# Optimization experiments

Measured on AMD Instinct MI355X. Metric: run time of the kernel, lower is better.

Reference implementation:

```python
import jax, jax.numpy as jnp
import numpy as np

SLOPE = 25.0   # fast_sigmoid surrogate slope (affects backward only)
THRESH = 1.0   # snntorch Leaky default threshold

@jax.custom_vjp
def spike(x):
    # Heaviside forward, fast-sigmoid surrogate backward
    return (x > 0).astype(x.dtype)

def _spike_fwd(x):
    return spike(x), x

def _spike_bwd(x, g):
    return (g / (SLOPE * jnp.abs(x) + 1.0) ** 2,)

spike.defvjp(_spike_fwd, _spike_bwd)


def setup_inputs() -> dict:
    key = jax.random.key(0)
    ks = jax.random.split(key, 16)
    B, T, F = 512, 1024, 64
    SNN, H, HOR = 128, 128, 24
    s = 0.05
    inp = {
        "x": jax.random.normal(ks[0], (B, T, F), jnp.float32),
        "proj_w": jax.random.normal(ks[1], (SNN, F), jnp.float32) * s,
        "proj_b": jnp.zeros((SNN,), jnp.float32),
        "beta1": jnp.full((SNN,), 0.9, jnp.float32),
        "beta2": jnp.full((SNN,), 0.9, jnp.float32),
        "gru_w_ih": jax.random.normal(ks[2], (3 * H, F + SNN), jnp.float32) * s,
        "gru_w_hh": jax.random.normal(ks[3], (3 * H, H), jnp.float32) * s,
        "gru_b_ih": jnp.zeros((3 * H,), jnp.float32),
        "gru_b_hh": jnp.zeros((3 * H,), jnp.float32),
        "attn_w1": jax.random.normal(ks[4], (H // 2, H), jnp.float32) * s,
        "attn_b1": jnp.zeros((H // 2,), jnp.float32),
        "attn_w2": jax.random.normal(ks[5], (1, H // 2), jnp.float32) * s,
        "attn_b2": jnp.zeros((1,), jnp.float32),
        "head_w": jax.random.normal(ks[6], (HOR, H), jnp.float32) * s,
        "head_b": jnp.zeros((HOR,), jnp.float32),
    }
    return inp


def reference(x, proj_w, proj_b, beta1, beta2,
              gru_w_ih, gru_w_hh, gru_b_ih, gru_b_hh,
              attn_w1, attn_b1, attn_w2, attn_b2, head_w, head_b):
    b1 = jnp.clip(beta1, 0.0, 0.99)
    b2 = jnp.clip(beta2, 0.0, 0.99)

    delta = x[:, 1:, :] - x[:, :-1, :]   # (B, T-1, F)
    raw = x[:, 1:, :]
    h_s = delta @ proj_w.T + proj_b      # (B, T-1, SNN)

    B = x.shape[0]
    SNN = proj_w.shape[0]

    # snntorch Leaky (subtract reset, reset from previous step's spike):
    # mem_t = beta*mem_{t-1} + in_t - spk_{t-1}*thr ; spk_t = H(mem_t - thr)
    def snn_step(carry, inp_t):
        m1, s1, m2, s2 = carry
        m1 = b1 * m1 + inp_t - s1 * THRESH
        s1n = spike(m1 - THRESH)
        m2 = b2 * m2 + s1n - s2 * THRESH
        s2n = spike(m2 - THRESH)
        return (m1, s1n, m2, s2n), m2

    z = jnp.zeros((B, SNN), x.dtype)
    _, mem_rec = jax.lax.scan(snn_step, (z, z, z, z), jnp.swapaxes(h_s, 0, 1))
    h_snn = jnp.swapaxes(mem_rec, 0, 1)             # (B, T-1, SNN)

    h_comb = jnp.concatenate([raw, h_snn], axis=-1)  # (B, T-1, F+SNN)

    # GRU (PyTorch gate layout: r, z, n)
    H = gru_w_hh.shape[1]
    x_proj = h_comb @ gru_w_ih.T + gru_b_ih          # (B, T-1, 3H)

    def gru_step(h, xp):
        gh = h @ gru_w_hh.T + gru_b_hh
        xr, xz, xn = jnp.split(xp, 3, axis=-1)
        hr, hz, hn = jnp.split(gh, 3, axis=-1)
        r = jax.nn.sigmoid(xr + hr)
        zg = jax.nn.sigmoid(xz + hz)
        n = jnp.tanh(xn + r * hn)
        h_new = (1.0 - zg) * n + zg * h
        return h_new, h_new

    h0 = jnp.zeros((B, H), x.dtype)
    _, gru_seq = jax.lax.scan(gru_step, h0, jnp.swapaxes(x_proj, 0, 1))
    gru_out = jnp.swapaxes(gru_seq, 0, 1)            # (B, T-1, H)

    # Temporal attention over time (dim=1)
    scores = jax.nn.relu(gru_out @ attn_w1.T + attn_b1) @ attn_w2.T + attn_b2  # (B, T-1, 1)
    w = jax.nn.softmax(scores, axis=1)
    h_ann = (w * gru_out).sum(axis=1)                # (B, H)

    return h_ann @ head_w.T + head_b                 # (B, horizon)
```

## Files before the change

### kernel.cpp

```cpp
#include <hip/hip_runtime.h>

typedef unsigned short u16;
typedef __attribute__((ext_vector_type(8))) short short8;
typedef __attribute__((ext_vector_type(4))) float f32x4;

__device__ __forceinline__ u16 f2bf(float f) {
  union { float f; unsigned u; } v; v.f = f;
  unsigned r = v.u + 0x7fffu + ((v.u >> 16) & 1u);
  return (u16)(r >> 16);
}
__device__ __forceinline__ u16 truncbf(float f) {
  union { float f; unsigned u; } v; v.f = f;
  return (u16)(v.u >> 16);
}
__device__ __forceinline__ float bf2f(u16 h) {
  union { unsigned u; float f; } v; v.u = ((unsigned)h) << 16;
  return v.f;
}
__device__ __forceinline__ void gll16(const void* g, void* l) {
  __builtin_amdgcn_global_load_lds((const __attribute__((address_space(1))) unsigned*)g,
                                   (__attribute__((address_space(3))) unsigned*)l, 16, 0, 0);
}
__device__ __forceinline__ void bar_lds() {
  asm volatile("s_waitcnt lgkmcnt(0)" ::: "memory");
  __builtin_amdgcn_s_barrier();
  asm volatile("" ::: "memory");
}

#define BATCH 512
#define TS 1023
#define NF 64
#define NS 128
#define NH 128
#define NG 384
#define NC 192
#define CH 128

__global__ void k_prep(const float* __restrict__ wih, const float* __restrict__ w1,
                       u16* __restrict__ wihb, u16* __restrict__ w1b) {
  int i = blockIdx.x * 256 + threadIdx.x;
  if (i < NG * NC) wihb[i] = f2bf(wih[i]);
  if (i < 64 * NH) w1b[i] = f2bf(w1[i]);
}

__global__ __launch_bounds__(256, 2) void k_front(const float* __restrict__ x,
                                                  const float* __restrict__ pw,
                                                  const float* __restrict__ pb,
                                                  const float* __restrict__ beta1,
                                                  const float* __restrict__ beta2,
                                                  u16* __restrict__ hcomb) {
  __shared__ float hst[64 * 138];
  const int tid = threadIdx.x, lane = tid & 63, w = tid >> 6;
  const int m16 = lane & 15, quad = lane >> 4;
  const int b = blockIdx.x;
  const float* xb = x + (long)b * 65536;

  const int tm = (w >> 1) * 32, nn = (w & 1) * 64;

  short8 bh[2][4], bl[2][4];
  #pragma unroll
  for (int kc = 0; kc < 2; ++kc)
    #pragma unroll
    for (int ni = 0; ni < 4; ++ni) {
      const float* src = pw + (nn + ni * 16 + m16) * 64 + kc * 32 + quad * 8;
      f32x4 v0 = *(const f32x4*)src;
      f32x4 v1 = *(const f32x4*)(src + 4);
      #pragma unroll
      for (int jj = 0; jj < 8; ++jj) {
        float v = (jj < 4) ? v0[jj & 3] : v1[jj & 3];
        u16 hh = truncbf(v);
        bh[kc][ni][jj] = (short)hh;
        bl[kc][ni][jj] = (short)f2bf(v - bf2f(hh));
      }
    }

  float b1v = 0.f, b2v = 0.f, m1 = 0.f, s1 = 0.f, m2 = 0.f, s2 = 0.f;
  if (tid < 128) {
    b1v = fminf(fmaxf(beta1[tid], 0.f), 0.99f);
    b2v = fminf(fmaxf(beta2[tid], 0.f), 0.99f);
  }
  float pbv[4];
  #pragma unroll
  for (int ni = 0; ni < 4; ++ni) pbv[ni] = pb[nn + ni * 16 + m16];

  for (int tile = 0; tile < 16; ++tile) {
    const int t0 = tile * 64;
    const int tl = (TS - t0 < 64) ? (TS - t0) : 64;

    f32x4 acc[2][4] = {};
    #pragma unroll
    for (int kc = 0; kc < 2; ++kc) {
      short8 ah[2], al[2];
      #pragma unroll
      for (int mi = 0; mi < 2; ++mi) {
        int row = tm + mi * 16 + m16;
        int tA = t0 + row; if (tA > 1022) tA = 1022;
        const float* p0 = xb + (long)tA * 64 + kc * 32 + quad * 8;
        f32x4 lo0 = *(const f32x4*)p0;
        f32x4 lo1 = *(const f32x4*)(p0 + 4);
        f32x4 hi0 = *(const f32x4*)(p0 + 64);
        f32x4 hi1 = *(const f32x4*)(p0 + 68);
        float d[8];
        #pragma unroll
        for (int jj = 0; jj < 4; ++jj) { d[jj] = hi0[jj] - lo0[jj]; d[4 + jj] = hi1[jj] - lo1[jj]; }
        #pragma unroll
        for (int jj = 0; jj < 8; ++jj) {
          u16 hh = truncbf(d[jj]);
          ah[mi][jj] = (short)hh;
          al[mi][jj] = (short)f2bf(d[jj] - bf2f(hh));
        }
      }
      #pragma unroll
      for (int mi = 0; mi < 2; ++mi)
        #pragma unroll
        for (int ni = 0; ni < 4; ++ni) {
          acc[mi][ni] = __builtin_amdgcn_mfma_f32_16x16x32_bf16(ah[mi], bh[kc][ni], acc[mi][ni], 0, 0, 0);
          acc[mi][ni] = __builtin_amdgcn_mfma_f32_16x16x32_bf16(ah[mi], bl[kc][ni], acc[mi][ni], 0, 0, 0);
          acc[mi][ni] = __builtin_amdgcn_mfma_f32_16x16x32_bf16(al[mi], bh[kc][ni], acc[mi][ni], 0, 0, 0);
        }
    }
    #pragma unroll
    for (int mi = 0; mi < 2; ++mi)
      #pragma unroll
      for (int ni = 0; ni < 4; ++ni)
        #pragma unroll
        for (int rr = 0; rr < 4; ++rr)
          hst[(tm + mi * 16 + quad * 4 + rr) * 138 + nn + ni * 16 + m16] = acc[mi][ni][rr] + pbv[ni];
    bar_lds();
    if (tid < 128) {
      const int n = tid;
      u16* dst = hcomb + ((long)t0 * 512 + b) * NC + 64 + n;
      for (int tt = 0; tt < tl; tt += 8) {
        float v[8];
        #pragma unroll
        for (int jj = 0; jj < 8; ++jj) {
          int t = tt + jj; if (t > 63) t = 63;
          v[jj] = hst[t * 138 + n];
        }
        #pragma unroll
        for (int jj = 0; jj < 8; ++jj) {
          int t = tt + jj;
          if (t < tl) {
            m1 = b1v * m1 + v[jj] - s1;
            s1 = (m1 > 1.0f) ? 1.0f : 0.0f;
            m2 = b2v * m2 + s1 - s2;
            s2 = (m2 > 1.0f) ? 1.0f : 0.0f;
            dst[(long)t * (512 * NC)] = f2bf(m2);
          }
        }
      }
    } else {
      const int f = tid & 63, half = (tid >> 6) & 1;
      for (int r = half; r < tl; r += 2)
        hcomb[((long)(t0 + r) * 512 + b) * NC + f] = f2bf(xb[(long)(t0 + r + 1) * 64 + f]);
    }
    bar_lds();
  }
}

__device__ __forceinline__ void xproj_body(long row0, int n0, const u16* __restrict__ hc,
                                           const u16* __restrict__ wih, const float* __restrict__ bih,
                                           u16* __restrict__ xp, u16* As, u16* Bs) {
  const int tid = threadIdx.x, lane = tid & 63, w = tid >> 6;
  const int m16 = lane & 15, quad = lane >> 4;
  const int wm = (w >> 1) * 64, wn = (w & 1) * 64;
  f32x4 acc[4][4] = {};
  const char* gA = (const char*)hc + (row0 + (lane >> 2)) * (NC * 2) + (lane & 3) * 16;
  const char* gB = (const char*)wih + (long)(n0 + (lane >> 2)) * (NC * 2) + (lane & 3) * 16;
  for (int kc = 0; kc < 6; ++kc) {
    #pragma unroll
    for (int i = 0; i < 2; ++i) {
      int q = i * 4 + w;
      gll16(gA + (long)q * 16 * (NC * 2) + kc * 64, (char*)As + q * 1024);
      gll16(gB + (long)q * 16 * (NC * 2) + kc * 64, (char*)Bs + q * 1024);
    }
    __syncthreads();
    short8 af[4], bfr[4];
    #pragma unroll
    for (int mi = 0; mi < 4; ++mi) af[mi] = *(const short8*)((const char*)As + (wm + mi * 16 + m16) * 64 + quad * 16);
    #pragma unroll
    for (int ni = 0; ni < 4; ++ni) bfr[ni] = *(const short8*)((const char*)Bs + (wn + ni * 16 + m16) * 64 + quad * 16);
    #pragma unroll
    for (int mi = 0; mi < 4; ++mi)
      #pragma unroll
      for (int ni = 0; ni < 4; ++ni)
        acc[mi][ni] = __builtin_amdgcn_mfma_f32_16x16x32_bf16(af[mi], bfr[ni], acc[mi][ni], 0, 0, 0);
    __syncthreads();
  }
  #pragma unroll
  for (int ni = 0; ni < 4; ++ni) {
    int n = n0 + wn + ni * 16 + m16;
    float bias = bih[n];
    #pragma unroll
    for (int mi = 0; mi < 4; ++mi) {
      long r = row0 + wm + mi * 16 + quad * 4;
      #pragma unroll
      for (int rr = 0; rr < 4; ++rr)
        xp[(r + rr) * NG + n] = f2bf(acc[mi][ni][rr] + bias);
    }
  }
}

__global__ __launch_bounds__(256) void k_xproj(const u16* __restrict__ hc, const u16* __restrict__ wih,
                                               const float* __restrict__ bih, u16* __restrict__ xp) {
  __shared__ alignas(16) u16 As[4096], Bs[4096];
  xproj_body((long)blockIdx.x * 128, blockIdx.y * 128, hc, wih, bih, xp, As, Bs);
}

__device__ __forceinline__ void score_body(long row0, const u16* __restrict__ gbf, const u16* __restrict__ w1,
                                           const float* __restrict__ b1, const float* __restrict__ w2,
                                           const float* __restrict__ b2, float* __restrict__ scores,
                                           u16* Gs, u16* Ws) {
  const int tid = threadIdx.x, lane = tid & 63, w = tid >> 6;
  const int m16 = lane & 15, quad = lane >> 4;
  f32x4 acc[2][4] = {};
  const char* gG = (const char*)gbf + (row0 + (lane >> 2)) * (NH * 2) + (lane & 3) * 16;
  const char* gW = (const char*)w1 + (long)(w * 16 + (lane >> 2)) * (NH * 2) + (lane & 3) * 16;
  for (int kc = 0; kc < 4; ++kc) {
    #pragma unroll
    for (int i = 0; i < 2; ++i) {
      int q = i * 4 + w;
      gll16(gG + (long)q * 16 * (NH * 2) + kc * 64, (char*)Gs + q * 1024);
    }
    gll16(gW + kc * 64, (char*)Ws + w * 1024);
    __syncthreads();
    short8 af[2], bfr[4];
    #pragma unroll
    for (int mi = 0; mi < 2; ++mi) af[mi] = *(const short8*)((const char*)Gs + (w * 32 + mi * 16 + m16) * 64 + quad * 16);
    #pragma unroll
    for (int ni = 0; ni < 4; ++ni) bfr[ni] = *(const short8*)((const char*)Ws + (ni * 16 + m16) * 64 + quad * 16);
    #pragma unroll
    for (int mi = 0; mi < 2; ++mi)
      #pragma unroll
      for (int ni = 0; ni < 4; ++ni)
        acc[mi][ni] = __builtin_amdgcn_mfma_f32_16x16x32_bf16(af[mi], bfr[ni], acc[mi][ni], 0, 0, 0);
    __syncthreads();
  }
  float b2v = b2[0];
  float w2v[4], b1v[4];
  #pragma unroll
  for (int ni = 0; ni < 4; ++ni) { w2v[ni] = w2[ni * 16 + m16]; b1v[ni] = b1[ni * 16 + m16]; }
  #pragma unroll
  for (int mi = 0; mi < 2; ++mi) {
    #pragma unroll
    for (int rr = 0; rr < 4; ++rr) {
      float v = 0.f;
      #pragma unroll
      for (int ni = 0; ni < 4; ++ni) {
        float hv = acc[mi][ni][rr] + b1v[ni];
        hv = hv > 0.f ? hv : 0.f;
        v = fmaf(hv, w2v[ni], v);
      }
      v += __shfl_xor(v, 1, 64); v += __shfl_xor(v, 2, 64);
      v += __shfl_xor(v, 4, 64); v += __shfl_xor(v, 8, 64);
      if (m16 == 0) scores[row0 + w * 32 + mi * 16 + quad * 4 + rr] = v + b2v;
    }
  }
}

__global__ __launch_bounds__(256) void k_score(const u16* __restrict__ gbf, const u16* __restrict__ w1,
                                               const float* __restrict__ b1, const float* __restrict__ w2,
                                               const float* __restrict__ b2, float* __restrict__ scores,
                                               long row_base) {
  __shared__ alignas(16) u16 Gs[4096], Ws[2048];
  score_body(row_base + (long)blockIdx.x * 128, gbf, w1, b1, w2, b2, scores, Gs, Ws);
}

__global__ __launch_bounds__(256, 2) void k_gru(const u16* __restrict__ xp, const float* __restrict__ whh,
                                                const float* __restrict__ bhh, u16* __restrict__ gout,
                                                float* __restrict__ h_state, int first, int nsteps,
                                                const u16* __restrict__ hcN, const u16* __restrict__ wihb,
                                                const float* __restrict__ bih, u16* __restrict__ xpN,
                                                int nxr, int nxp,
                                                const u16* __restrict__ gbf, const u16* __restrict__ w1,
                                                const float* __restrict__ b1, const float* __restrict__ w2,
                                                const float* __restrict__ b2, float* __restrict__ scores,
                                                long score_base) {
  __shared__ alignas(16) u16 frag[2 * 2048];
  __shared__ alignas(16) u16 smem[8192];
  if (blockIdx.x >= 256) {
    int ebid = blockIdx.x - 256;
    if (ebid < nxp)
      xproj_body((long)(ebid % nxr) * 128, (ebid / nxr) * 128, hcN, wihb, bih, xpN, smem, smem + 4096);
    else
      score_body(score_base + (long)(ebid - nxp) * 128, gbf, w1, b1, w2, b2, scores, smem, smem + 4096);
    return;
  }
  const int tid = threadIdx.x, lane = tid & 63, w = tid >> 6;
  const int m16 = lane & 15, quad = lane >> 4;
  const long bg0 = (long)blockIdx.x * 2;
  {
    short8 z8 = {};
    *(short8*)((char*)frag + tid * 16) = z8;
    *(short8*)((char*)frag + 4096 + tid * 16) = z8;
  }
  short8 wf[6][4];
  #pragma unroll
  for (int g = 0; g < 3; ++g)
    #pragma unroll
    for (int hh = 0; hh < 2; ++hh)
      #pragma unroll
      for (int c = 0; c < 4; ++c) {
        const float* src = whh + (long)(g * 128 + 32 * w + hh * 16 + m16) * NH + c * 32 + quad * 8;
        short8 v;
        #pragma unroll
        for (int jj = 0; jj < 8; ++jj) v[jj] = (short)f2bf(src[jj]);
        wf[g * 2 + hh][c] = v;
      }
  const int bq = quad & 1, hq = quad >> 1;
  const int j = 32 * w + hq * 16 + m16;
  const long brow = bg0 + bq;
  const float br_ = bhh[j], bz_ = bhh[128 + j], bn_ = bhh[256 + j];
  float h = first ? 0.f : h_state[brow * NH + j];
  const int fragoff = w * 1024 + 64 * bq + 256 * (hq * 2 + (m16 >> 3)) + 2 * (m16 & 7);
  __syncthreads();
  {
    u16 hb0 = f2bf(h);
    *(u16*)((char*)frag + fragoff) = hb0;
    *(u16*)((char*)frag + fragoff + 128) = hb0;
  }
  const u16* xbase = xp + brow * NG + j;
  u16 pr[8], pz[8], pn[8], sbuf[8];
  #pragma unroll
  for (int u = 0; u < 8; ++u) {
    const u16* xr = xbase + (long)u * (512 * NG);
    pr[u] = xr[0]; pz[u] = xr[128]; pn[u] = xr[256];
  }
  __syncthreads();

#define GRU_STEP(T, U)                                                                     \
  {                                                                                        \
    const int cur = ((T) & 1) * 4096, nxt = 4096 - cur;                                    \
    short8 af[4];                                                                          \
    _Pragma("unroll")                                                                      \
    for (int c = 0; c < 4; ++c)                                                            \
      af[c] = *(const short8*)((const char*)frag + cur + c * 1024 + lane * 16);            \
    f32x4 zero = {0.f, 0.f, 0.f, 0.f};                                                     \
    f32x4 accA[6], accB[6];                                                                \
    _Pragma("unroll")                                                                      \
    for (int nt = 0; nt < 6; ++nt) {                                                       \
      accA[nt] = __builtin_amdgcn_mfma_f32_16x16x32_bf16(af[0], wf[nt][0], zero, 0, 0, 0); \
      accB[nt] = __builtin_amdgcn_mfma_f32_16x16x32_bf16(af[2], wf[nt][2], zero, 0, 0, 0); \
    }                                                                                      \
    _Pragma("unroll")                                                                      \
    for (int nt = 0; nt < 6; ++nt) {                                                       \
      accA[nt] = __builtin_amdgcn_mfma_f32_16x16x32_bf16(af[1], wf[nt][1], accA[nt], 0, 0, 0); \
      accB[nt] = __builtin_amdgcn_mfma_f32_16x16x32_bf16(af[3], wf[nt][3], accB[nt], 0, 0, 0); \
    }                                                                                      \
    float ghr = (hq ? (accA[1][0] + accB[1][0]) : (accA[0][0] + accB[0][0])) + br_;        \
    float ghz = (hq ? (accA[3][0] + accB[3][0]) : (accA[2][0] + accB[2][0])) + bz_;        \
    float ghn = (hq ? (accA[5][0] + accB[5][0]) : (accA[4][0] + accB[4][0])) + bn_;        \
    float xrv = bf2f(pr[U]), xzv = bf2f(pz[U]), xnv = bf2f(pn[U]);                         \
    float rg = 1.f / (1.f + __expf(-(xrv + ghr)));                                         \
    float zg = 1.f / (1.f + __expf(-(xzv + ghz)));                                         \
    float niv = xnv + rg * ghn;                                                            \
    float ng = 1.f - 2.f / (1.f + __expf(2.f * niv));                                      \
    h = (1.f - zg) * ng + zg * h;                                                          \
    u16 hb = f2bf(h);                                                                      \
    sbuf[U] = hb;                                                                          \
    *(u16*)((char*)frag + nxt + fragoff) = hb;                                             \
    *(u16*)((char*)frag + nxt + fragoff + 128) = hb;                                       \
    __syncthreads();                                                                       \
  }

  const int N8 = nsteps & ~7;
  for (int t8 = 0; t8 < N8; t8 += 8) {
    if (t8 > 0) {
      #pragma unroll
      for (int u = 0; u < 8; ++u)
        gout[((long)(t8 - 8 + u) * 512 + brow) * NH + j] = sbuf[u];
    }
    u16 npr[8], npz[8], npn[8];
    #pragma unroll
    for (int u = 0; u < 8; ++u) {
      long tp = t8 + 8 + u; if (tp > nsteps - 1) tp = nsteps - 1;
      const u16* xr = xbase + tp * (512 * NG);
      npr[u] = xr[0]; npz[u] = xr[128]; npn[u] = xr[256];
    }
    GRU_STEP(t8 + 0, 0) GRU_STEP(t8 + 1, 1) GRU_STEP(t8 + 2, 2) GRU_STEP(t8 + 3, 3)
    GRU_STEP(t8 + 4, 4) GRU_STEP(t8 + 5, 5) GRU_STEP(t8 + 6, 6) GRU_STEP(t8 + 7, 7)
    #pragma unroll
    for (int u = 0; u < 8; ++u) { pr[u] = npr[u]; pz[u] = npz[u]; pn[u] = npn[u]; }
  }
  #pragma unroll
  for (int u = 0; u < 8; ++u)
    gout[((long)(N8 - 8 + u) * 512 + brow) * NH + j] = sbuf[u];
  const int tail = nsteps & 7;
  #pragma unroll
  for (int u = 0; u < 7; ++u) {
    if (u < tail) {
      GRU_STEP(N8 + u, u)
      gout[((long)(N8 + u) * 512 + brow) * NH + j] = sbuf[u];
    }
  }
#undef GRU_STEP
  h_state[brow * NH + j] = h;
}

__global__ __launch_bounds__(256) void k_attn(const float* __restrict__ scores, const u16* __restrict__ gout,
                                              const float* __restrict__ headw, const float* __restrict__ headb,
                                              float* __restrict__ out) {
  __shared__ float sc[TS];
  __shared__ float red[8];
  __shared__ float part[8][132];
  __shared__ float hann[128];
  const int tid = threadIdx.x, lane = tid & 63, w = tid >> 6;
  const long b = blockIdx.x;
  const float* srow = scores + b;
  float s0[4];
  #pragma unroll
  for (int i = 0; i < 4; ++i) {
    int t = tid + i * 256;
    s0[i] = (t < TS) ? srow[(long)t * 512] : -1e30f;
  }
  float mx = fmaxf(fmaxf(s0[0], s0[1]), fmaxf(s0[2], s0[3]));
  #pragma unroll
  for (int off = 32; off > 0; off >>= 1) mx = fmaxf(mx, __shfl_xor(mx, off, 64));
  if (lane == 0) red[w] = mx;
  __syncthreads();
  mx = fmaxf(fmaxf(red[0], red[1]), fmaxf(red[2], red[3]));
  float sum = 0.f;
  #pragma unroll
  for (int i = 0; i < 4; ++i) {
    int t = tid + i * 256;
    if (t < TS) { float e = __expf(s0[i] - mx); sc[t] = e; sum += e; }
  }
  #pragma unroll
  for (int off = 32; off > 0; off >>= 1) sum += __shfl_xor(sum, off, 64);
  if (lane == 0) red[4 + w] = sum;
  __syncthreads();
  float inv = 1.f / (red[4] + red[5] + red[6] + red[7]);
  const int jg = tid & 31, sl = tid >> 5;
  float acc[4] = {0.f, 0.f, 0.f, 0.f};
  const u16* gbase = gout + b * NH + jg * 4;
  for (int t = sl; t < TS; t += 8) {
    float wt = sc[t];
    ushort4 g4 = *(const ushort4*)(gbase + (long)t * (512 * NH));
    acc[0] = fmaf(wt, bf2f(g4.x), acc[0]);
    acc[1] = fmaf(wt, bf2f(g4.y), acc[1]);
    acc[2] = fmaf(wt, bf2f(g4.z), acc[2]);
    acc[3] = fmaf(wt, bf2f(g4.w), acc[3]);
  }
  #pragma unroll
  for (int i = 0; i < 4; ++i) part[sl][jg * 4 + i] = acc[i];
  __syncthreads();
  if (tid < 128) {
    float v = 0.f;
    #pragma unroll
    for (int s = 0; s < 8; ++s) v += part[s][tid];
    hann[tid] = v * inv;
  }
  __syncthreads();
  if (tid < 24) {
    float a = headb[tid];
    const float* hwr = headw + tid * 128;
    for (int k = 0; k < 128; k += 4) {
      float4 h4 = *(const float4*)&hann[k];
      float4 w4 = *(const float4*)&hwr[k];
      a = fmaf(h4.x, w4.x, a); a = fmaf(h4.y, w4.y, a);
      a = fmaf(h4.z, w4.z, a); a = fmaf(h4.w, w4.w, a);
    }
    out[b * 24 + tid] = a;
  }
}

extern "C" void kernel_launch(void* const* d_in, const int* in_sizes, int n_in,
                              void* d_out, int out_size, void* d_ws, size_t ws_size,
                              hipStream_t stream) {
  const float* x      = (const float*)d_in[0];
  const float* proj_w = (const float*)d_in[1];
  const float* proj_b = (const float*)d_in[2];
  const float* beta1  = (const float*)d_in[3];
  const float* beta2  = (const float*)d_in[4];
  const float* gwih   = (const float*)d_in[5];
  const float* gwhh   = (const float*)d_in[6];
  const float* gbih   = (const float*)d_in[7];
  const float* gbhh   = (const float*)d_in[8];
  const float* aw1    = (const float*)d_in[9];
  const float* ab1    = (const float*)d_in[10];
  const float* aw2    = (const float*)d_in[11];
  const float* ab2    = (const float*)d_in[12];
  const float* hw     = (const float*)d_in[13];
  const float* hb     = (const float*)d_in[14];
  float* out = (float*)d_out;
  char* ws = (char*)d_ws;

  u16*   hcomb  = (u16*)(ws);
  u16*   xpbuf  = (u16*)(ws + 201129984L);
  u16*   gru    = (u16*)(ws + 335216640L);
  float* scores = (float*)(ws + 469303296L);
  u16*   wihb   = (u16*)(ws + 471398400L);
  u16*   w1b    = (u16*)(ws + 471545856L);
  float* hstate = (float*)(ws + 471562240L);

  u16* slot[2] = {xpbuf, xpbuf + 25165824L};

  k_prep<<<288, 256, 0, stream>>>(gwih, aw1, wihb, w1b);
  k_front<<<512, 256, 0, stream>>>(x, proj_w, proj_b, beta1, beta2, hcomb);
  k_xproj<<<dim3(512, 3), 256, 0, stream>>>(hcomb, wihb, gbih, slot[0]);
  for (int c = 0; c < 8; ++c) {
    int len = (c == 7) ? 127 : 128;
    long start = (long)c * CH;
    int lenN = (c + 1 == 7) ? 127 : 128;
    int nxr = (c < 7) ? (lenN * 512 / 128) : 0;
    int nxp = nxr * 3;
    int nsc = (c >= 1) ? 512 : 0;
    const u16* hcN = hcomb + (start + len) * 512L * NC;
    long score_base = (c >= 1) ? ((long)(c - 1) * CH * 512) : 0;
    k_gru<<<256 + nxp + nsc, 256, 0, stream>>>(
        slot[c & 1], gwhh, gbhh, gru + start * 512L * NH, hstate, c == 0 ? 1 : 0, len,
        hcN, wihb, gbih, slot[(c + 1) & 1], nxr, nxp,
        gru, w1b, ab1, aw2, ab2, scores, score_base);
  }
  k_score<<<508, 256, 0, stream>>>(gru, w1b, ab1, aw2, ab2, scores, 896L * 512);
  k_attn<<<512, 256, 0, stream>>>(scores, gru, hw, hb, out);
}
```

Measured before the change: 964.8 us.

## Stage x tiles in swizzled LDS and prefetch next tile during SNN scan

k_front now copies each 65-row x tile into an XOR-swizzled LDS buffer once. The delta MFMA operands are then read from LDS instead of loading every row twice from global memory. The next tile's global loads are issued into registers before the serial SNN recurrence and written to LDS afterwards, so memory latency overlaps with the scan. This costs about 17KB more LDS per block, 20 extra staging VGPRs, and a moved barrier that occupancy and correctness now depend on.

```diff
diff --git a/kernel.cpp b/kernel.cpp
--- a/kernel.cpp
+++ b/kernel.cpp
@@ -50,12 +50,35 @@
                                                   const float* __restrict__ beta2,
                                                   u16* __restrict__ hcomb) {
   __shared__ float hst[64 * 138];
+  __shared__ alignas(16) float xs[17 * 256];
   const int tid = threadIdx.x, lane = tid & 63, w = tid >> 6;
   const int m16 = lane & 15, quad = lane >> 4;
   const int b = blockIdx.x;
   const float* xb = x + (long)b * 65536;
+  const char* xsb = (const char*)xs;
 
   const int tm = (w >> 1) * 32, nn = (w & 1) * 64;
+
+  f32x4 stg[5];
+  auto stage_load = [&](int tt0, int rws) {
+    const int total = rws * 16;
+    #pragma unroll
+    for (int i = 0; i < 5; ++i) {
+      int g = tid + i * 256;
+      if (g < total) stg[i] = *(const f32x4*)((const char*)xb + (long)tt0 * 256 + (long)g * 16);
+    }
+  };
+  auto stage_write = [&](int rws) {
+    const int total = rws * 16;
+    #pragma unroll
+    for (int i = 0; i < 5; ++i) {
+      int g = tid + i * 256;
+      if (g < total) {
+        int row = g >> 4, ch = g & 15;
+        *(f32x4*)((char*)xs + row * 256 + ((ch ^ (row & 7)) << 4)) = stg[i];
+      }
+    }
+  };
 
   short8 bh[2][4], bl[2][4];
   #pragma unroll
@@ -83,9 +106,13 @@
   #pragma unroll
   for (int ni = 0; ni < 4; ++ni) pbv[ni] = pb[nn + ni * 16 + m16];
 
+  stage_load(0, 65);
+  stage_write(65);
+
   for (int tile = 0; tile < 16; ++tile) {
     const int t0 = tile * 64;
     const int tl = (TS - t0 < 64) ? (TS - t0) : 64;
+    bar_lds();
 
     f32x4 acc[2][4] = {};
     #pragma unroll
@@ -93,13 +120,13 @@
       short8 ah[2], al[2];
       #pragma unroll
       for (int mi = 0; mi < 2; ++mi) {
-        int row = tm + mi * 16 + m16;
-        int tA = t0 + row; if (tA > 1022) tA = 1022;
-        const float* p0 = xb + (long)tA * 64 + kc * 32 + quad * 8;
-        f32x4 lo0 = *(const f32x4*)p0;
-        f32x4 lo1 = *(const f32x4*)(p0 + 4);
-        f32x4 hi0 = *(const f32x4*)(p0 + 64);
-        f32x4 hi1 = *(const f32x4*)(p0 + 68);
+        int r = tm + mi * 16 + m16;
+        int cb = kc * 8 + quad * 2;
+        int r7 = r & 7, r71 = (r + 1) & 7;
+        f32x4 lo0 = *(const f32x4*)(xsb + r * 256 + ((cb ^ r7) << 4));
+        f32x4 lo1 = *(const f32x4*)(xsb + r * 256 + (((cb + 1) ^ r7) << 4));
+        f32x4 hi0 = *(const f32x4*)(xsb + (r + 1) * 256 + ((cb ^ r71) << 4));
+        f32x4 hi1 = *(const f32x4*)(xsb + (r + 1) * 256 + (((cb + 1) ^ r71) << 4));
         float d[8];
         #pragma unroll
         for (int jj = 0; jj < 4; ++jj) { d[jj] = hi0[jj] - lo0[jj]; d[4 + jj] = hi1[jj] - lo1[jj]; }
@@ -127,6 +154,9 @@
         for (int rr = 0; rr < 4; ++rr)
           hst[(tm + mi * 16 + quad * 4 + rr) * 138 + nn + ni * 16 + m16] = acc[mi][ni][rr] + pbv[ni];
     bar_lds();
+    const int nt0 = t0 + 64;
+    const int nrws = (1024 - nt0 < 65) ? (1024 - nt0) : 65;
+    if (tile < 15) stage_load(nt0, nrws);
     if (tid < 128) {
       const int n = tid;
       u16* dst = hcomb + ((long)t0 * 512 + b) * NC + 64 + n;
@@ -154,7 +184,7 @@
       for (int r = half; r < tl; r += 2)
         hcomb[((long)(t0 + r) * 512 + b) * NC + f] = f2bf(xb[(long)(t0 + r + 1) * 64 + f]);
     }
-    bar_lds();
+    if (tile < 15) stage_write(nrws);
   }
 }
 
```

After: 998.6 us. +3.5%, slower.
